# Performance work log

Hardware: AMD Instinct MI355X
Metric: run time of the kernel (lower is better)

## Reference

```python
import jax, jax.numpy as jnp
import numpy as np

N, C, E = 50000, 128, 400000
R_CUT = 5.0


def setup_inputs() -> dict:
    key = jax.random.key(0)
    ks = jax.random.split(key, 12)
    s = jax.random.normal(ks[0], (N, C), dtype=jnp.float32)
    v = jax.random.normal(ks[1], (N, 3, C), dtype=jnp.float32)
    edges = jax.random.randint(ks[2], (E, 2), 0, N, dtype=jnp.int64)
    r_ij = jax.random.uniform(ks[3], (E, 1), dtype=jnp.float32, minval=0.1, maxval=R_CUT)
    rn = jax.random.normal(ks[4], (E, 3), dtype=jnp.float32)
    r_ij_normalized = rn / jnp.linalg.norm(rn, axis=-1, keepdims=True)
    sc = 1.0 / np.sqrt(C)
    W1 = jax.random.normal(ks[5], (C, C), dtype=jnp.float32) * sc
    b1 = jnp.zeros((C,), dtype=jnp.float32)
    W2 = jax.random.normal(ks[6], (C, 3 * C), dtype=jnp.float32) * sc
    b2 = jnp.zeros((3 * C,), dtype=jnp.float32)
    Wr = jax.random.normal(ks[7], (20, 3 * C), dtype=jnp.float32) * (1.0 / np.sqrt(20))
    br = jnp.zeros((3 * C,), dtype=jnp.float32)
    return {"s": s, "v": v, "edges": edges, "r_ij": r_ij,
            "r_ij_normalized": r_ij_normalized,
            "W1": W1, "b1": b1, "W2": W2, "b2": b2, "Wr": Wr, "br": br}


def rbf(r_ij, r_cut):
    # r_ij: [E,1] -> [E,20]; sin(n*pi/r_cut * r) / r for n=1..20
    n = jnp.arange(1, 21, dtype=r_ij.dtype)  # [20]
    return jnp.sin((np.pi / r_cut) * n * r_ij) / r_ij


def fcut(r_ij, r_cut):
    return 0.5 * (jnp.cos(np.pi * r_ij / r_cut) + 1.0)  # [E,1]


def reference(s, v, edges, r_ij, r_ij_normalized, W1, b1, W2, b2, Wr, br):
    r_cut = R_CUT
    src = edges[:, 1]
    dst = edges[:, 0]
    # RBF filter: [E,3C], modulated by cosine cutoff
    rbf_pass = (rbf(r_ij, r_cut) @ Wr + br) * fcut(r_ij, r_cut)
    # node MLP: Linear -> SiLU -> Linear : [N,3C]
    s_pass = jax.nn.silu(s @ W1 + b1) @ W2 + b2
    pass_out = rbf_pass * s_pass[src]  # [E,3C]
    dv, ds, drep = jnp.split(pass_out, 3, axis=-1)  # each [E,C]
    # [E,3,C] = gathered v * gate + direction * rep
    delta_v = v[src] * dv[:, None, :] + r_ij_normalized[:, :, None] * drep[:, None, :]
    s_out = s + jax.ops.segment_sum(ds, dst, num_segments=N)
    v_out = v + jax.ops.segment_sum(delta_v, dst, num_segments=N)
    return s_out, v_out
```

## Files before the change

### kernel.cpp

```cpp
#include <hip/hip_runtime.h>
#include <hip/hip_bf16.h>

#define CC 128
#define NOUT 384
#define PI_F 3.14159265358979323846f
#define RCUT 5.0f

__device__ __forceinline__ float loadF(const void* p, size_t i, int isf32) {
  if (isf32) return ((const float*)p)[i];
  unsigned int w = ((unsigned int)((const unsigned short*)p)[i]) << 16;
  return __uint_as_float(w);
}
__device__ __forceinline__ int loadI(const void* p, size_t i, int isi64) {
  if (isi64) return (int)((const long long*)p)[i];
  return ((const int*)p)[i];
}

__global__ void detect_kernel(const void* s, const void* edges, int* flags) {
  if (threadIdx.x == 0) {
    int isf32 = 0;
    const unsigned short* us = (const unsigned short*)s;
    for (int i = 0; i < 1024; i++) {
      unsigned int w = ((unsigned int)us[i]) << 16;
      float f = __uint_as_float(w);
      if (!(fabsf(f) < 1000.f)) { isf32 = 1; break; }
    }
    int isi64 = 1;
    const int* ie = (const int*)edges;
    for (int i = 1; i < 128; i += 2) {
      if (ie[i] != 0) { isi64 = 0; break; }
    }
    flags[0] = isf32;
    flags[1] = isi64;
  }
}

__global__ void count_kernel(const void* __restrict__ edges, int* __restrict__ cnt,
                             const int* __restrict__ flags, int E) {
  int e = blockIdx.x * blockDim.x + threadIdx.x;
  if (e >= E) return;
  int dst = loadI(edges, (size_t)2 * e, flags[1]);
  atomicAdd(&cnt[dst], 1);
}

__global__ __launch_bounds__(1024) void scan_kernel(const int* __restrict__ cnt,
                                                    int* __restrict__ row_start,
                                                    int* __restrict__ next, int N) {
  __shared__ int woff[16];
  __shared__ int carry_sh;
  const int t = threadIdx.x;
  const int lane = t & 63;
  const int wid = t >> 6;
  if (t == 0) carry_sh = 0;
  __syncthreads();
  for (int base = 0; base < N; base += 1024) {
    int x = (base + t < N) ? cnt[base + t] : 0;
    int incl = x;
    #pragma unroll
    for (int off = 1; off < 64; off <<= 1) {
      int y = __shfl_up(incl, off, 64);
      if (lane >= off) incl += y;
    }
    if (lane == 63) woff[wid] = incl;
    __syncthreads();
    if (wid == 0 && lane < 16) {
      int w = woff[lane];
      int iw = w;
      #pragma unroll
      for (int off = 1; off < 16; off <<= 1) {
        int y = __shfl_up(iw, off, 64);
        if (lane >= off) iw += y;
      }
      woff[lane] = iw - w;
    }
    __syncthreads();
    int carry = carry_sh;
    int excl = carry + woff[wid] + incl - x;
    if (base + t < N) { row_start[base + t] = excl; next[base + t] = excl; }
    __syncthreads();
    if (t == 1023) carry_sh = excl + x;
    __syncthreads();
  }
  if (t == 0) row_start[N] = carry_sh;
}

template <int PRE>
__global__ void fill_kernel(const void* __restrict__ edges,
                            const void* __restrict__ r_ij,
                            const void* __restrict__ rn,
                            int* __restrict__ next,
                            int* __restrict__ esrc,
                            float4* __restrict__ efcrn,
                            float* __restrict__ erb,
                            const int* __restrict__ flags, int E) {
  int e = blockIdx.x * blockDim.x + threadIdx.x;
  if (e >= E) return;
  const int isi64 = flags[1];
  const int isf32 = flags[0];
  const int dst = loadI(edges, (size_t)2 * e, isi64);
  const int src = loadI(edges, (size_t)2 * e + 1, isi64);
  const float r  = loadF(r_ij, e, isf32);
  const float r0 = loadF(rn, (size_t)e * 3 + 0, isf32);
  const float r1 = loadF(rn, (size_t)e * 3 + 1, isf32);
  const float r2 = loadF(rn, (size_t)e * 3 + 2, isf32);
  const int p = atomicAdd(&next[dst], 1);
  esrc[p] = src;
  efcrn[p] = make_float4(r, r0, r1, r2);
  if (PRE) {
    const float x = (PI_F / RCUT) * r;
    const float s1 = __sinf(x);
    const float c1 = __cosf(x);
    const float rinv = __builtin_amdgcn_rcpf(r);
    const float twoc = 2.f * c1;
    float sp = 0.f, sn = s1;
    float rbv[20];
    #pragma unroll
    for (int k = 0; k < 20; k++) {
      rbv[k] = sn * rinv;
      const float s2 = twoc * sn - sp;
      sp = sn; sn = s2;
    }
    float4* rb4 = (float4*)(erb + (size_t)p * 20);
    #pragma unroll
    for (int j = 0; j < 5; j++)
      rb4[j] = make_float4(rbv[4 * j], rbv[4 * j + 1], rbv[4 * j + 2], rbv[4 * j + 3]);
  }
}

template <int ISF32>
__device__ __forceinline__ void node_mlp_body(
    const void* __restrict__ s,
    const void* __restrict__ W1, const void* __restrict__ b1,
    const void* __restrict__ W2, const void* __restrict__ b2,
    __hip_bfloat16* __restrict__ s_pass, int N) {
  const int M = 8;
  __shared__ float s_sh[M][CC];
  __shared__ float h_sh[M][CC];
  const int c = threadIdx.x;
  const int n0 = blockIdx.x * M;

  #pragma unroll
  for (int m = 0; m < M; m++) {
    int n = n0 + m;
    s_sh[m][c] = (n < N) ? loadF(s, (size_t)n * CC + c, ISF32) : 0.f;
  }
  __syncthreads();

  float acc[M];
  #pragma unroll
  for (int m = 0; m < M; m++) acc[m] = 0.f;
  for (int k = 0; k < CC; k++) {
    float w = loadF(W1, (size_t)k * CC + c, ISF32);
    #pragma unroll
    for (int m = 0; m < M; m++) acc[m] += s_sh[m][k] * w;
  }
  float bb1 = loadF(b1, c, ISF32);
  #pragma unroll
  for (int m = 0; m < M; m++) {
    float x = acc[m] + bb1;
    h_sh[m][c] = x / (1.f + __expf(-x));
  }
  __syncthreads();

  #pragma unroll
  for (int jj = 0; jj < 3; jj++) {
    int j = jj * CC + c;
    float a2[M];
    #pragma unroll
    for (int m = 0; m < M; m++) a2[m] = 0.f;
    for (int k = 0; k < CC; k++) {
      float w = loadF(W2, (size_t)k * NOUT + j, ISF32);
      #pragma unroll
      for (int m = 0; m < M; m++) a2[m] += h_sh[m][k] * w;
    }
    float bb2 = loadF(b2, j, ISF32);
    #pragma unroll
    for (int m = 0; m < M; m++) {
      int n = n0 + m;
      if (n < N) s_pass[(size_t)n * NOUT + j] = __float2bfloat16(a2[m] + bb2);
    }
  }
}

__global__ __launch_bounds__(128) void node_mlp_kernel(
    const void* __restrict__ s,
    const void* __restrict__ W1, const void* __restrict__ b1,
    const void* __restrict__ W2, const void* __restrict__ b2,
    __hip_bfloat16* __restrict__ s_pass, const int* __restrict__ flags, int N) {
  if (flags[0]) node_mlp_body<1>(s, W1, b1, W2, b2, s_pass, N);
  else          node_mlp_body<0>(s, W1, b1, W2, b2, s_pass, N);
}

template <int ISF32, int PRE>
__device__ __forceinline__ void agg_body(
    const void* __restrict__ s, const void* __restrict__ v,
    const void* __restrict__ Wr, const void* __restrict__ br,
    const __hip_bfloat16* __restrict__ s_pass,
    const int* __restrict__ row_start,
    const int* __restrict__ esrc, const float4* __restrict__ efcrn,
    const float* __restrict__ erb,
    void* __restrict__ out, int N) {
  const int n = blockIdx.x;
  const int c = threadIdx.x;

  float w0[20], w1[20], w2[20];
  #pragma unroll
  for (int k = 0; k < 20; k++) {
    w0[k] = loadF(Wr, (size_t)k * NOUT + c, ISF32);
    w1[k] = loadF(Wr, (size_t)k * NOUT + CC + c, ISF32);
    w2[k] = loadF(Wr, (size_t)k * NOUT + 2 * CC + c, ISF32);
  }
  const float b0  = loadF(br, c, ISF32);
  const float b1v = loadF(br, CC + c, ISF32);
  const float b2v = loadF(br, 2 * CC + c, ISF32);

  float accs = 0.f, av0 = 0.f, av1 = 0.f, av2 = 0.f;
  const int beg = row_start[n], end = row_start[n + 1];
  for (int i = beg; i < end; ++i) {
    const int src = esrc[i];
    const float4 fr = efcrn[i];
    const size_t sb = (size_t)src * NOUT;

    const float sp0 = __bfloat162float(s_pass[sb + c]);
    const float sp1 = __bfloat162float(s_pass[sb + CC + c]);
    const float sp2 = __bfloat162float(s_pass[sb + 2 * CC + c]);
    float vv0, vv1, vv2;
    if (ISF32) {
      const float* vf = (const float*)v;
      vv0 = vf[sb + c];
      vv1 = vf[sb + CC + c];
      vv2 = vf[sb + 2 * CC + c];
    } else {
      const unsigned short* vb = (const unsigned short*)v;
      vv0 = __uint_as_float(((unsigned int)vb[sb + c]) << 16);
      vv1 = __uint_as_float(((unsigned int)vb[sb + CC + c]) << 16);
      vv2 = __uint_as_float(((unsigned int)vb[sb + 2 * CC + c]) << 16);
    }

    const float fc = 0.5f * (__cosf((PI_F / RCUT) * fr.x) + 1.f);

    float a0 = b0, a1 = b1v, a2 = b2v;
    if (PRE) {
      const float4* rb4 = (const float4*)(erb + (size_t)i * 20);
      #pragma unroll
      for (int j = 0; j < 5; j++) {
        const float4 rb = rb4[j];
        a0 += rb.x * w0[4 * j];     a1 += rb.x * w1[4 * j];     a2 += rb.x * w2[4 * j];
        a0 += rb.y * w0[4 * j + 1]; a1 += rb.y * w1[4 * j + 1]; a2 += rb.y * w2[4 * j + 1];
        a0 += rb.z * w0[4 * j + 2]; a1 += rb.z * w1[4 * j + 2]; a2 += rb.z * w2[4 * j + 2];
        a0 += rb.w * w0[4 * j + 3]; a1 += rb.w * w1[4 * j + 3]; a2 += rb.w * w2[4 * j + 3];
      }
    } else {
      const float x = (PI_F / RCUT) * fr.x;
      const float s1 = __sinf(x);
      const float c1 = __cosf(x);
      const float rinv = __builtin_amdgcn_rcpf(fr.x);
      const float twoc = 2.f * c1;
      float sp = 0.f, sn = s1;
      #pragma unroll
      for (int k = 0; k < 20; k++) {
        const float rb = sn * rinv;
        a0 += rb * w0[k]; a1 += rb * w1[k]; a2 += rb * w2[k];
        const float s2 = twoc * sn - sp;
        sp = sn; sn = s2;
      }
    }

    const float p0 = a0 * fc * sp0;
    const float p1 = a1 * fc * sp1;
    const float p2 = a2 * fc * sp2;
    accs += p1;
    av0 += vv0 * p0 + fr.y * p2;
    av1 += vv1 * p0 + fr.z * p2;
    av2 += vv2 * p0 + fr.w * p2;
  }

  const size_t si = (size_t)n * CC + c;
  const size_t vi = (size_t)n * NOUT;
  const float so = loadF(s, si, ISF32) + accs;
  float o0, o1, o2;
  if (ISF32) {
    const float* vf = (const float*)v;
    o0 = vf[vi + 0 * CC + c] + av0;
    o1 = vf[vi + 1 * CC + c] + av1;
    o2 = vf[vi + 2 * CC + c] + av2;
  } else {
    const unsigned short* vb = (const unsigned short*)v;
    o0 = __uint_as_float(((unsigned int)vb[vi + 0 * CC + c]) << 16) + av0;
    o1 = __uint_as_float(((unsigned int)vb[vi + 1 * CC + c]) << 16) + av1;
    o2 = __uint_as_float(((unsigned int)vb[vi + 2 * CC + c]) << 16) + av2;
  }
  const size_t vo = (size_t)N * CC + vi;
  if (ISF32) {
    float* o = (float*)out;
    o[si] = so;
    o[vo + 0 * CC + c] = o0;
    o[vo + 1 * CC + c] = o1;
    o[vo + 2 * CC + c] = o2;
  } else {
    __hip_bfloat16* o = (__hip_bfloat16*)out;
    o[si] = __float2bfloat16(so);
    o[vo + 0 * CC + c] = __float2bfloat16(o0);
    o[vo + 1 * CC + c] = __float2bfloat16(o1);
    o[vo + 2 * CC + c] = __float2bfloat16(o2);
  }
}

template <int PRE>
__global__ __launch_bounds__(128, 3) void aggregate_kernel(
    const void* __restrict__ s, const void* __restrict__ v,
    const void* __restrict__ Wr, const void* __restrict__ br,
    const __hip_bfloat16* __restrict__ s_pass,
    const int* __restrict__ row_start,
    const int* __restrict__ esrc, const float4* __restrict__ efcrn,
    const float* __restrict__ erb,
    void* __restrict__ out, const int* __restrict__ flags, int N) {
  if (flags[0]) agg_body<1, PRE>(s, v, Wr, br, s_pass, row_start, esrc, efcrn, erb, out, N);
  else          agg_body<0, PRE>(s, v, Wr, br, s_pass, row_start, esrc, efcrn, erb, out, N);
}

extern "C" void kernel_launch(void* const* d_in, const int* in_sizes, int n_in,
                              void* d_out, int out_size, void* d_ws, size_t ws_size,
                              hipStream_t stream) {
  const void* s     = d_in[0];
  const void* v     = d_in[1];
  const void* edges = d_in[2];
  const void* r_ij  = d_in[3];
  const void* rn    = d_in[4];
  const void* W1    = d_in[5];
  const void* b1    = d_in[6];
  const void* W2    = d_in[7];
  const void* b2    = d_in[8];
  const void* Wr    = d_in[9];
  const void* br    = d_in[10];

  const int N = in_sizes[0] / CC;
  const int E = in_sizes[3];

  char* ws = (char*)d_ws;
  int* flags = (int*)ws;
  size_t off = 256;
  __hip_bfloat16* s_pass = (__hip_bfloat16*)(ws + off);
  off += (size_t)N * NOUT * sizeof(__hip_bfloat16);
  float4* efcrn = (float4*)(ws + off);   off += (size_t)E * sizeof(float4);
  int* esrc      = (int*)(ws + off);     off += (size_t)E * sizeof(int);
  int* cnt       = (int*)(ws + off);     off += (size_t)N * sizeof(int);
  int* row_start = (int*)(ws + off);     off += (size_t)(N + 1) * sizeof(int);
  int* next      = (int*)(ws + off);     off += (size_t)N * sizeof(int);
  off = (off + 15) & ~(size_t)15;
  float* erb = (float*)(ws + off);
  const size_t need_pre = off + (size_t)E * 20 * sizeof(float);
  const int pre = (ws_size >= need_pre) ? 1 : 0;

  hipMemsetAsync(cnt, 0, (size_t)N * sizeof(int), stream);

  detect_kernel<<<1, 64, 0, stream>>>(s, edges, flags);
  count_kernel<<<(E + 255) / 256, 256, 0, stream>>>(edges, cnt, flags, E);
  scan_kernel<<<1, 1024, 0, stream>>>(cnt, row_start, next, N);
  if (pre)
    fill_kernel<1><<<(E + 255) / 256, 256, 0, stream>>>(edges, r_ij, rn, next,
                                                        esrc, efcrn, erb, flags, E);
  else
    fill_kernel<0><<<(E + 255) / 256, 256, 0, stream>>>(edges, r_ij, rn, next,
                                                        esrc, efcrn, erb, flags, E);
  node_mlp_kernel<<<(N + 7) / 8, 128, 0, stream>>>(s, W1, b1, W2, b2, s_pass,
                                                   flags, N);
  if (pre)
    aggregate_kernel<1><<<N, 128, 0, stream>>>(s, v, Wr, br, s_pass, row_start,
                                               esrc, efcrn, erb, d_out, flags, N);
  else
    aggregate_kernel<0><<<N, 128, 0, stream>>>(s, v, Wr, br, s_pass, row_start,
                                               esrc, efcrn, erb, d_out, flags, N);
}
```

Baseline: 660.6 us.

## Pack node MLP output with v[:,0] into per-channel uint2 table; pair-unroll edge loop

The node MLP now writes a packed bf16 table per node and channel holding the three s_pass outputs plus the first v component. This makes one 8-byte gather per edge replace three scattered bf16 loads and one v load. The cosine cutoff is folded into the precomputed RBF values in the fill kernel, so fcut is no longer recomputed per edge. The aggregate loop processes two edges per iteration using packed float2 FMAs to expose more memory-level parallelism. The cost is that v[:,0] is rounded to bf16, which loses precision, and register pressure rises.

```diff
diff --git a/kernel.cpp b/kernel.cpp
--- a/kernel.cpp
+++ b/kernel.cpp
@@ -6,6 +6,8 @@
 #define PI_F 3.14159265358979323846f
 #define RCUT 5.0f
 
+typedef float f32x2 __attribute__((ext_vector_type(2)));
+
 __device__ __forceinline__ float loadF(const void* p, size_t i, int isf32) {
   if (isf32) return ((const float*)p)[i];
   unsigned int w = ((unsigned int)((const unsigned short*)p)[i]) << 16;
@@ -14,6 +16,21 @@
 __device__ __forceinline__ int loadI(const void* p, size_t i, int isi64) {
   if (isi64) return (int)((const long long*)p)[i];
   return ((const int*)p)[i];
+}
+__device__ __forceinline__ unsigned int bfbits(float f) {
+  __hip_bfloat16 h = __float2bfloat16(f);
+  unsigned short u;
+  __builtin_memcpy(&u, &h, 2);
+  return (unsigned int)u;
+}
+__device__ __forceinline__ unsigned int bfpack(float lo, float hi) {
+  return bfbits(lo) | (bfbits(hi) << 16);
+}
+__device__ __forceinline__ float bf16lo(unsigned int u) {
+  return __uint_as_float(u << 16);
+}
+__device__ __forceinline__ float bf16hi(unsigned int u) {
+  return __uint_as_float(u & 0xffff0000u);
 }
 
 __global__ void detect_kernel(const void* s, const void* edges, int* flags) {
@@ -105,18 +122,19 @@
   const float r2 = loadF(rn, (size_t)e * 3 + 2, isf32);
   const int p = atomicAdd(&next[dst], 1);
   esrc[p] = src;
-  efcrn[p] = make_float4(r, r0, r1, r2);
   if (PRE) {
     const float x = (PI_F / RCUT) * r;
     const float s1 = __sinf(x);
     const float c1 = __cosf(x);
-    const float rinv = __builtin_amdgcn_rcpf(r);
+    const float fc = 0.5f * (c1 + 1.f);
+    efcrn[p] = make_float4(fc, r0, r1, r2);
+    const float rf = __builtin_amdgcn_rcpf(r) * fc;
     const float twoc = 2.f * c1;
     float sp = 0.f, sn = s1;
     float rbv[20];
     #pragma unroll
     for (int k = 0; k < 20; k++) {
-      rbv[k] = sn * rinv;
+      rbv[k] = sn * rf;
       const float s2 = twoc * sn - sp;
       sp = sn; sn = s2;
     }
@@ -124,15 +142,17 @@
     #pragma unroll
     for (int j = 0; j < 5; j++)
       rb4[j] = make_float4(rbv[4 * j], rbv[4 * j + 1], rbv[4 * j + 2], rbv[4 * j + 3]);
+  } else {
+    efcrn[p] = make_float4(r, r0, r1, r2);
   }
 }
 
 template <int ISF32>
 __device__ __forceinline__ void node_mlp_body(
-    const void* __restrict__ s,
+    const void* __restrict__ s, const void* __restrict__ v,
     const void* __restrict__ W1, const void* __restrict__ b1,
     const void* __restrict__ W2, const void* __restrict__ b2,
-    __hip_bfloat16* __restrict__ s_pass, int N) {
+    uint2* __restrict__ tabA, int N) {
   const int M = 8;
   __shared__ float s_sh[M][CC];
   __shared__ float h_sh[M][CC];
@@ -162,6 +182,7 @@
   }
   __syncthreads();
 
+  float a2s[3][M];
   #pragma unroll
   for (int jj = 0; jj < 3; jj++) {
     int j = jj * CC + c;
@@ -175,27 +196,33 @@
     }
     float bb2 = loadF(b2, j, ISF32);
     #pragma unroll
-    for (int m = 0; m < M; m++) {
-      int n = n0 + m;
-      if (n < N) s_pass[(size_t)n * NOUT + j] = __float2bfloat16(a2[m] + bb2);
-    }
+    for (int m = 0; m < M; m++) a2s[jj][m] = a2[m] + bb2;
+  }
+
+  #pragma unroll
+  for (int m = 0; m < M; m++) {
+    int n = n0 + m;
+    if (n >= N) continue;
+    const float v0 = loadF(v, (size_t)n * NOUT + c, ISF32);
+    const size_t tix = (size_t)n * CC + c;
+    tabA[tix] = make_uint2(bfpack(a2s[0][m], a2s[1][m]), bfpack(a2s[2][m], v0));
   }
 }
 
 __global__ __launch_bounds__(128) void node_mlp_kernel(
-    const void* __restrict__ s,
+    const void* __restrict__ s, const void* __restrict__ v,
     const void* __restrict__ W1, const void* __restrict__ b1,
     const void* __restrict__ W2, const void* __restrict__ b2,
-    __hip_bfloat16* __restrict__ s_pass, const int* __restrict__ flags, int N) {
-  if (flags[0]) node_mlp_body<1>(s, W1, b1, W2, b2, s_pass, N);
-  else          node_mlp_body<0>(s, W1, b1, W2, b2, s_pass, N);
+    uint2* __restrict__ tabA, const int* __restrict__ flags, int N) {
+  if (flags[0]) node_mlp_body<1>(s, v, W1, b1, W2, b2, tabA, N);
+  else          node_mlp_body<0>(s, v, W1, b1, W2, b2, tabA, N);
 }
 
 template <int ISF32, int PRE>
 __device__ __forceinline__ void agg_body(
     const void* __restrict__ s, const void* __restrict__ v,
     const void* __restrict__ Wr, const void* __restrict__ br,
-    const __hip_bfloat16* __restrict__ s_pass,
+    const uint2* __restrict__ tabA,
     const int* __restrict__ row_start,
     const int* __restrict__ esrc, const float4* __restrict__ efcrn,
     const float* __restrict__ erb,
@@ -203,12 +230,15 @@
   const int n = blockIdx.x;
   const int c = threadIdx.x;
 
-  float w0[20], w1[20], w2[20];
-  #pragma unroll
-  for (int k = 0; k < 20; k++) {
-    w0[k] = loadF(Wr, (size_t)k * NOUT + c, ISF32);
-    w1[k] = loadF(Wr, (size_t)k * NOUT + CC + c, ISF32);
-    w2[k] = loadF(Wr, (size_t)k * NOUT + 2 * CC + c, ISF32);
+  f32x2 w0p[10], w1p[10], w2p[10];
+  #pragma unroll
+  for (int j = 0; j < 10; j++) {
+    w0p[j] = f32x2{loadF(Wr, (size_t)(2 * j) * NOUT + c, ISF32),
+                   loadF(Wr, (size_t)(2 * j + 1) * NOUT + c, ISF32)};
+    w1p[j] = f32x2{loadF(Wr, (size_t)(2 * j) * NOUT + CC + c, ISF32),
+                   loadF(Wr, (size_t)(2 * j + 1) * NOUT + CC + c, ISF32)};
+    w2p[j] = f32x2{loadF(Wr, (size_t)(2 * j) * NOUT + 2 * CC + c, ISF32),
+                   loadF(Wr, (size_t)(2 * j + 1) * NOUT + 2 * CC + c, ISF32)};
   }
   const float b0  = loadF(br, c, ISF32);
   const float b1v = loadF(br, CC + c, ISF32);
@@ -216,80 +246,145 @@
 
   float accs = 0.f, av0 = 0.f, av1 = 0.f, av2 = 0.f;
   const int beg = row_start[n], end = row_start[n + 1];
-  for (int i = beg; i < end; ++i) {
+
+  int i = beg;
+  for (; i + 2 <= end; i += 2) {
+    const int srcA = esrc[i];
+    const int srcB = esrc[i + 1];
+    const float4 frA = efcrn[i];
+    const float4 frB = efcrn[i + 1];
+    const uint2 taA = tabA[(size_t)srcA * CC + c];
+    const uint2 taB = tabA[(size_t)srcB * CC + c];
+    const float v1A = loadF(v, (size_t)srcA * NOUT + CC + c, ISF32);
+    const float v2A = loadF(v, (size_t)srcA * NOUT + 2 * CC + c, ISF32);
+    const float v1B = loadF(v, (size_t)srcB * NOUT + CC + c, ISF32);
+    const float v2B = loadF(v, (size_t)srcB * NOUT + 2 * CC + c, ISF32);
+
+    float fcA, fcB;
+    f32x2 rbA[10], rbB[10];
+    if (PRE) {
+      fcA = frA.x;
+      fcB = frB.x;
+      const f32x2* rpA = (const f32x2*)(erb + (size_t)i * 20);
+      const f32x2* rpB = (const f32x2*)(erb + (size_t)(i + 1) * 20);
+      #pragma unroll
+      for (int j = 0; j < 10; j++) { rbA[j] = rpA[j]; rbB[j] = rpB[j]; }
+    } else {
+      const float xA = (PI_F / RCUT) * frA.x;
+      const float s1A = __sinf(xA), c1A = __cosf(xA);
+      fcA = 0.5f * (c1A + 1.f);
+      const float rfA = __builtin_amdgcn_rcpf(frA.x) * fcA;
+      const float twocA = 2.f * c1A;
+      const float xB = (PI_F / RCUT) * frB.x;
+      const float s1B = __sinf(xB), c1B = __cosf(xB);
+      fcB = 0.5f * (c1B + 1.f);
+      const float rfB = __builtin_amdgcn_rcpf(frB.x) * fcB;
+      const float twocB = 2.f * c1B;
+      float spA = 0.f, snA = s1A, spB = 0.f, snB = s1B;
+      #pragma unroll
+      for (int j = 0; j < 10; j++) {
+        const float qA0 = snA * rfA;
+        float s2 = twocA * snA - spA; spA = snA; snA = s2;
+        const float qA1 = snA * rfA;
+        s2 = twocA * snA - spA; spA = snA; snA = s2;
+        rbA[j] = f32x2{qA0, qA1};
+        const float qB0 = snB * rfB;
+        s2 = twocB * snB - spB; spB = snB; snB = s2;
+        const float qB1 = snB * rfB;
+        s2 = twocB * snB - spB; spB = snB; snB = s2;
+        rbB[j] = f32x2{qB0, qB1};
+      }
+    }
+
+    f32x2 a0A = f32x2{0.f, 0.f}, a1A = a0A, a2A = a0A;
+    f32x2 a0B = a0A, a1B = a0A, a2B = a0A;
+    #pragma unroll
+    for (int j = 0; j < 10; j++) {
+      a0A += rbA[j] * w0p[j];  a0B += rbB[j] * w0p[j];
+      a1A += rbA[j] * w1p[j];  a1B += rbB[j] * w1p[j];
+      a2A += rbA[j] * w2p[j];  a2B += rbB[j] * w2p[j];
+    }
+
+    const float a0Af = fmaf(b0,  fcA, a0A.x + a0A.y);
+    const float a1Af = fmaf(b1v, fcA, a1A.x + a1A.y);
+    const float a2Af = fmaf(b2v, fcA, a2A.x + a2A.y);
+    const float p0A = a0Af * bf16lo(taA.x);
+    const float p1A = a1Af * bf16hi(taA.x);
+    const float p2A = a2Af * bf16lo(taA.y);
+    accs += p1A;
+    av0 = fmaf(bf16hi(taA.y), p0A, fmaf(frA.y, p2A, av0));
+    av1 = fmaf(v1A, p0A, fmaf(frA.z, p2A, av1));
+    av2 = fmaf(v2A, p0A, fmaf(frA.w, p2A, av2));
+
+    const float a0Bf = fmaf(b0,  fcB, a0B.x + a0B.y);
+    const float a1Bf = fmaf(b1v, fcB, a1B.x + a1B.y);
+    const float a2Bf = fmaf(b2v, fcB, a2B.x + a2B.y);
+    const float p0B = a0Bf * bf16lo(taB.x);
+    const float p1B = a1Bf * bf16hi(taB.x);
+    const float p2B = a2Bf * bf16lo(taB.y);
+    accs += p1B;
+    av0 = fmaf(bf16hi(taB.y), p0B, fmaf(frB.y, p2B, av0));
+    av1 = fmaf(v1B, p0B, fmaf(frB.z, p2B, av1));
+    av2 = fmaf(v2B, p0B, fmaf(frB.w, p2B, av2));
+  }
+
+  for (; i < end; ++i) {
     const int src = esrc[i];
     const float4 fr = efcrn[i];
-    const size_t sb = (size_t)src * NOUT;
-
-    const float sp0 = __bfloat162float(s_pass[sb + c]);
-    const float sp1 = __bfloat162float(s_pass[sb + CC + c]);
-    const float sp2 = __bfloat162float(s_pass[sb + 2 * CC + c]);
-    float vv0, vv1, vv2;
-    if (ISF32) {
-      const float* vf = (const float*)v;
-      vv0 = vf[sb + c];
-      vv1 = vf[sb + CC + c];
-      vv2 = vf[sb + 2 * CC + c];
-    } else {
-      const unsigned short* vb = (const unsigned short*)v;
-      vv0 = __uint_as_float(((unsigned int)vb[sb + c]) << 16);
-      vv1 = __uint_as_float(((unsigned int)vb[sb + CC + c]) << 16);
-      vv2 = __uint_as_float(((unsigned int)vb[sb + 2 * CC + c]) << 16);
-    }
-
-    const float fc = 0.5f * (__cosf((PI_F / RCUT) * fr.x) + 1.f);
-
-    float a0 = b0, a1 = b1v, a2 = b2v;
+    const uint2 ta = tabA[(size_t)src * CC + c];
+    const float v1f = loadF(v, (size_t)src * NOUT + CC + c, ISF32);
+    const float v2f = loadF(v, (size_t)src * NOUT + 2 * CC + c, ISF32);
+
+    float fc;
+    f32x2 rb[10];
     if (PRE) {
-      const float4* rb4 = (const float4*)(erb + (size_t)i * 20);
-      #pragma unroll
-      for (int j = 0; j < 5; j++) {
-        const float4 rb = rb4[j];
-        a0 += rb.x * w0[4 * j];     a1 += rb.x * w1[4 * j];     a2 += rb.x * w2[4 * j];
-        a0 += rb.y * w0[4 * j + 1]; a1 += rb.y * w1[4 * j + 1]; a2 += rb.y * w2[4 * j + 1];
-        a0 += rb.z * w0[4 * j + 2]; a1 += rb.z * w1[4 * j + 2]; a2 += rb.z * w2[4 * j + 2];
-        a0 += rb.w * w0[4 * j + 3]; a1 += rb.w * w1[4 * j + 3]; a2 += rb.w * w2[4 * j + 3];
-      }
+      fc = fr.x;
+      const f32x2* rp = (const f32x2*)(erb + (size_t)i * 20);
+      #pragma unroll
+      for (int j = 0; j < 10; j++) rb[j] = rp[j];
     } else {
       const float x = (PI_F / RCUT) * fr.x;
-      const float s1 = __sinf(x);
-      const float c1 = __cosf(x);
-      const float rinv = __builtin_amdgcn_rcpf(fr.x);
+      const float s1 = __sinf(x), c1 = __cosf(x);
+      fc = 0.5f * (c1 + 1.f);
+      const float rf = __builtin_amdgcn_rcpf(fr.x) * fc;
       const float twoc = 2.f * c1;
-      float sp = 0.f, sn = s1;
-      #pragma unroll
-      for (int k = 0; k < 20; k++) {
-        const float rb = sn * rinv;
-        a0 += rb * w0[k]; a1 += rb * w1[k]; a2 += rb * w2[k];
-        const float s2 = twoc * sn - sp;
-        sp = sn; sn = s2;
+      float spv = 0.f, snv = s1;
+      #pragma unroll
+      for (int j = 0; j < 10; j++) {
+        const float q0 = snv * rf;
+        float s2 = twoc * snv - spv; spv = snv; snv = s2;
+        const float q1 = snv * rf;
+        s2 = twoc * snv - spv; spv = snv; snv = s2;
+        rb[j] = f32x2{q0, q1};
       }
     }
 
-    const float p0 = a0 * fc * sp0;
-    const float p1 = a1 * fc * sp1;
-    const float p2 = a2 * fc * sp2;
+    f32x2 a0p = f32x2{0.f, 0.f}, a1p = a0p, a2p = a0p;
+    #pragma unroll
+    for (int j = 0; j < 10; j++) {
+      a0p += rb[j] * w0p[j];
+      a1p += rb[j] * w1p[j];
+      a2p += rb[j] * w2p[j];
+    }
+
+    const float a0 = fmaf(b0,  fc, a0p.x + a0p.y);
+    const float a1 = fmaf(b1v, fc, a1p.x + a1p.y);
+    const float a2 = fmaf(b2v, fc, a2p.x + a2p.y);
+    const float p0 = a0 * bf16lo(ta.x);
+    const float p1 = a1 * bf16hi(ta.x);
+    const float p2 = a2 * bf16lo(ta.y);
     accs += p1;
-    av0 += vv0 * p0 + fr.y * p2;
-    av1 += vv1 * p0 + fr.z * p2;
-    av2 += vv2 * p0 + fr.w * p2;
+    av0 = fmaf(bf16hi(ta.y), p0, fmaf(fr.y, p2, av0));
+    av1 = fmaf(v1f, p0, fmaf(fr.z, p2, av1));
+    av2 = fmaf(v2f, p0, fmaf(fr.w, p2, av2));
   }
 
   const size_t si = (size_t)n * CC + c;
   const size_t vi = (size_t)n * NOUT;
   const float so = loadF(s, si, ISF32) + accs;
-  float o0, o1, o2;
-  if (ISF32) {
-    const float* vf = (const float*)v;
-    o0 = vf[vi + 0 * CC + c] + av0;
-    o1 = vf[vi + 1 * CC + c] + av1;
-    o2 = vf[vi + 2 * CC + c] + av2;
-  } else {
-    const unsigned short* vb = (const unsigned short*)v;
-    o0 = __uint_as_float(((unsigned int)vb[vi + 0 * CC + c]) << 16) + av0;
-    o1 = __uint_as_float(((unsigned int)vb[vi + 1 * CC + c]) << 16) + av1;
-    o2 = __uint_as_float(((unsigned int)vb[vi + 2 * CC + c]) << 16) + av2;
-  }
+  const float o0 = loadF(v, vi + 0 * CC + c, ISF32) + av0;
+  const float o1 = loadF(v, vi + 1 * CC + c, ISF32) + av1;
+  const float o2 = loadF(v, vi + 2 * CC + c, ISF32) + av2;
   const size_t vo = (size_t)N * CC + vi;
   if (ISF32) {
     float* o = (float*)out;
@@ -310,13 +405,13 @@
 __global__ __launch_bounds__(128, 3) void aggregate_kernel(
     const void* __restrict__ s, const void* __restrict__ v,
     const void* __restrict__ Wr, const void* __restrict__ br,
-    const __hip_bfloat16* __restrict__ s_pass,
+    const uint2* __restrict__ tabA,
     const int* __restrict__ row_start,
     const int* __restrict__ esrc, const float4* __restrict__ efcrn,
     const float* __restrict__ erb,
     void* __restrict__ out, const int* __restrict__ flags, int N) {
-  if (flags[0]) agg_body<1, PRE>(s, v, Wr, br, s_pass, row_start, esrc, efcrn, erb, out, N);
-  else          agg_body<0, PRE>(s, v, Wr, br, s_pass, row_start, esrc, efcrn, erb, out, N);
+  if (flags[0]) agg_body<1, PRE>(s, v, Wr, br, tabA, row_start, esrc, efcrn, erb, out, N);
+  else          agg_body<0, PRE>(s, v, Wr, br, tabA, row_start, esrc, efcrn, erb, out, N);
 }
 
 extern "C" void kernel_launch(void* const* d_in, const int* in_sizes, int n_in,
@@ -340,17 +435,16 @@
   char* ws = (char*)d_ws;
   int* flags = (int*)ws;
   size_t off = 256;
-  __hip_bfloat16* s_pass = (__hip_bfloat16*)(ws + off);
-  off += (size_t)N * NOUT * sizeof(__hip_bfloat16);
-  float4* efcrn = (float4*)(ws + off);   off += (size_t)E * sizeof(float4);
-  int* esrc      = (int*)(ws + off);     off += (size_t)E * sizeof(int);
-  int* cnt       = (int*)(ws + off);     off += (size_t)N * sizeof(int);
-  int* row_start = (int*)(ws + off);     off += (size_t)(N + 1) * sizeof(int);
-  int* next      = (int*)(ws + off);     off += (size_t)N * sizeof(int);
-  off = (off + 15) & ~(size_t)15;
+  auto align16 = [](size_t x) { return (x + 15) & ~(size_t)15; };
+  uint2* tabA = (uint2*)(ws + off);      off += align16((size_t)N * CC * 8);
+  float4* efcrn = (float4*)(ws + off);   off += align16((size_t)E * 16);
+  int* esrc = (int*)(ws + off);          off += align16((size_t)E * 4);
+  int* cnt = (int*)(ws + off);           off += align16((size_t)N * 4);
+  int* row_start = (int*)(ws + off);     off += align16((size_t)(N + 1) * 4);
+  int* next = (int*)(ws + off);          off += align16((size_t)N * 4);
   float* erb = (float*)(ws + off);
-  const size_t need_pre = off + (size_t)E * 20 * sizeof(float);
-  const int pre = (ws_size >= need_pre) ? 1 : 0;
+  const size_t off_erb_end = off + (size_t)E * 20 * 4;
+  const int pre = (ws_size >= off_erb_end) ? 1 : 0;
 
   hipMemsetAsync(cnt, 0, (size_t)N * sizeof(int), stream);
 
@@ -363,12 +457,12 @@
   else
     fill_kernel<0><<<(E + 255) / 256, 256, 0, stream>>>(edges, r_ij, rn, next,
                                                         esrc, efcrn, erb, flags, E);
-  node_mlp_kernel<<<(N + 7) / 8, 128, 0, stream>>>(s, W1, b1, W2, b2, s_pass,
-                                                   flags, N);
+  node_mlp_kernel<<<(N + 7) / 8, 128, 0, stream>>>(s, v, W1, b1, W2, b2,
+                                                   tabA, flags, N);
   if (pre)
-    aggregate_kernel<1><<<N, 128, 0, stream>>>(s, v, Wr, br, s_pass, row_start,
+    aggregate_kernel<1><<<N, 128, 0, stream>>>(s, v, Wr, br, tabA, row_start,
                                                esrc, efcrn, erb, d_out, flags, N);
   else
-    aggregate_kernel<0><<<N, 128, 0, stream>>>(s, v, Wr, br, s_pass, row_start,
+    aggregate_kernel<0><<<N, 128, 0, stream>>>(s, v, Wr, br, tabA, row_start,
                                                esrc, efcrn, erb, d_out, flags, N);
 }
```

After: 638.3 us. 1.03x faster.
